# Kernel tuning notes

Measured on AMD Instinct MI355X. Metric: run time of the kernel, lower is better.

The kernel has to match this reference:

```python
import jax, jax.numpy as jnp
import numpy as np

B, LF, RATE = 2, 2048, 4
DF, DS, H = 1024, 1024, 8
D2 = DF // 2            # 512: both self (d1) and cross (d2) branch dims (equal split)
POOL_H = 2048
TS = LF // RATE         # 512 slow steps


def _p(key, shape):
    return jax.random.normal(key, shape, jnp.float32) * 0.02


def setup_inputs() -> dict:
    keys = iter(jax.random.split(jax.random.key(0), 32))
    inp = {
        "x_fast": jax.random.normal(next(keys), (B, LF, DF), jnp.float32),
        "x_slow": jax.random.normal(next(keys), (B, TS, DS), jnp.float32),
    }
    for name in ("fself", "fcross", "sself", "scross"):
        inp[f"{name}_wqkv"] = _p(next(keys), (D2, 3 * D2))
        inp[f"{name}_bqkv"] = jnp.zeros((3 * D2,), jnp.float32)
        inp[f"{name}_wo"] = _p(next(keys), (D2, D2))
        inp[f"{name}_bo"] = jnp.zeros((D2,), jnp.float32)
    inp["lift_w"] = _p(next(keys), (DS, D2))
    inp["lift_b"] = jnp.zeros((D2,), jnp.float32)
    inp["pool_w1"] = _p(next(keys), (RATE * DF, POOL_H))
    inp["pool_b1"] = jnp.zeros((POOL_H,), jnp.float32)
    inp["pool_w2"] = _p(next(keys), (POOL_H, D2))
    inp["pool_b2"] = jnp.zeros((D2,), jnp.float32)
    return inp


def _mha(q_in, k_in, v_in, wqkv, bqkv, wo, bo):
    """Standard multihead attention with fused in-proj weight [d, 3d]."""
    b, tq, d = q_in.shape
    hd = d // H
    q = q_in @ wqkv[:, :d] + bqkv[:d]
    k = k_in @ wqkv[:, d:2 * d] + bqkv[d:2 * d]
    v = v_in @ wqkv[:, 2 * d:] + bqkv[2 * d:]
    q = q.reshape(b, tq, H, hd)
    k = k.reshape(b, k_in.shape[1], H, hd)
    v = v.reshape(b, v_in.shape[1], H, hd)
    scores = jnp.einsum('bqhd,bkhd->bhqk', q, k) * np.float32(1.0 / np.sqrt(hd))
    w = jax.nn.softmax(scores, axis=-1)
    o = jnp.einsum('bhqk,bkhd->bqhd', w, v).reshape(b, tq, d)
    return o @ wo + bo


def _forward(x_fast, x_slow,
             fself_wqkv, fself_bqkv, fself_wo, fself_bo,
             fcross_wqkv, fcross_bqkv, fcross_wo, fcross_bo,
             sself_wqkv, sself_bqkv, sself_wo, sself_bo,
             scross_wqkv, scross_bqkv, scross_wo, scross_bo,
             lift_w, lift_b, pool_w1, pool_b1, pool_w2, pool_b2):
    b = x_fast.shape[0]
    # ---- fast level: lift slow -> fast timescale (ffn applied before repeat)
    y = jnp.repeat(x_slow @ lift_w + lift_b, RATE, axis=1)          # [B, LF, D2]
    x1, x2 = x_fast[..., :D2], x_fast[..., D2:]
    z_fast = jnp.concatenate([
        _mha(x1, x1, x1, fself_wqkv, fself_bqkv, fself_wo, fself_bo),
        _mha(x2, y, y, fcross_wqkv, fcross_bqkv, fcross_wo, fcross_bo),
    ], axis=-1)
    # ---- slow level: causal block pooling of fast sequence
    blocks = x_fast.reshape(b, TS, RATE * DF)                        # LF == TS*RATE
    s = jax.nn.gelu(blocks @ pool_w1 + pool_b1) @ pool_w2 + pool_b2  # [B, TS, D2]
    # causal shift: prepend zero slow step, drop last (zero in pooled feature dim)
    s = jnp.concatenate([jnp.zeros((b, 1, D2), s.dtype), s[:, :-1]], axis=1)
    s1, s2 = x_slow[..., :D2], x_slow[..., D2:]
    z_slow = jnp.concatenate([
        _mha(s1, s1, s1, sself_wqkv, sself_bqkv, sself_wo, sself_bo),
        _mha(s2, s, s, scross_wqkv, scross_bqkv, scross_wo, scross_bo),
    ], axis=-1)
    return z_fast, z_slow


def reference(x_fast, x_slow,
              fself_wqkv, fself_bqkv, fself_wo, fself_bo,
              fcross_wqkv, fcross_bqkv, fcross_wo, fcross_bo,
              sself_wqkv, sself_bqkv, sself_wo, sself_bo,
              scross_wqkv, scross_bqkv, scross_wo, scross_bo,
              lift_w, lift_b, pool_w1, pool_b1, pool_w2, pool_b2):
    return _forward(x_fast, x_slow,
                    fself_wqkv, fself_bqkv, fself_wo, fself_bo,
                    fcross_wqkv, fcross_bqkv, fcross_wo, fcross_bo,
                    sself_wqkv, sself_bqkv, sself_wo, sself_bo,
                    scross_wqkv, scross_bqkv, scross_wo, scross_bo,
                    lift_w, lift_b, pool_w1, pool_b1, pool_w2, pool_b2)
```

## Files before the change

kernel.cpp:

```cpp
#include <hip/hip_runtime.h>
#include <hip/hip_bf16.h>


typedef __attribute__((ext_vector_type(8))) short bf16x8;
typedef __attribute__((ext_vector_type(4))) float f32x4;
typedef unsigned short u16;
typedef unsigned int u32;

__device__ inline u16 f2bf(float f) {
    __hip_bfloat16 h = __float2bfloat16(f);
    return *reinterpret_cast<u16*>(&h);
}
__device__ inline u32 pack2(float a, float b) {
    return (u32)f2bf(a) | ((u32)f2bf(b) << 16);
}
__device__ inline void gld16(const u16* g, u16* l) {
    __builtin_amdgcn_global_load_lds(
        (const __attribute__((address_space(1))) void*)(g),
        (__attribute__((address_space(3))) void*)(l), 16, 0, 0);
}

struct GDesc {
    const u16* A; const u16* Bt; const float* bias;
    void* out0; u16* aux0; u16* aux1;
    int lda, ldb, ldc, K, ntx, mode, rshift, tile_end;
};
struct GPack { int n; int pad[3]; GDesc d[8]; };

template <int TMT>
__global__ __launch_bounds__(256)
void gemm_multi(GPack pk)
{
    constexpr int TM = TMT * 16;
    constexpr int W = TMT / 2;
    __shared__ u16 As[TM * 64];
    __shared__ u16 Bs[TM * 64];

    int bid = blockIdx.x;
    int di = 0;
    while (bid >= pk.d[di].tile_end) ++di;
    const GDesc g = pk.d[di];
    const int base = di ? pk.d[di - 1].tile_end : 0;
    const int local = bid - base;
    const int ty = local / g.ntx, tx = local - ty * g.ntx;
    const int row0 = ty * TM, col0 = tx * TM;

    const int t = threadIdx.x;
    const int wave = t >> 6, lane = t & 63;
    const int l15 = lane & 15, quad = lane >> 4;
    const int wm = (wave >> 1) * W * 16, wn = (wave & 1) * W * 16;

    const int srow = wave * 8 + (lane >> 3);
    const int scol = (lane & 7) * 8;
    const u16* Ag = g.A + (long long)(row0 + srow) * g.lda + scol;
    const u16* Bg = g.Bt + (long long)(col0 + srow) * g.ldb + scol;

    f32x4 acc[W][W];
#pragma unroll
    for (int i = 0; i < W; ++i)
#pragma unroll
        for (int j = 0; j < W; ++j) {
            acc[i][j][0] = 0.f; acc[i][j][1] = 0.f;
            acc[i][j][2] = 0.f; acc[i][j][3] = 0.f;
        }

    for (int k0 = 0; k0 < g.K; k0 += 64) {
        __syncthreads();
#pragma unroll
        for (int r = 0; r < TM / 32; ++r) {
            gld16(Ag + (long long)r * 32 * g.lda + k0, As + r * 2048 + wave * 512);
            gld16(Bg + (long long)r * 32 * g.ldb + k0, Bs + r * 2048 + wave * 512);
        }
        __syncthreads();
#pragma unroll
        for (int kc = 0; kc < 2; ++kc) {
            bf16x8 af[W], bfr[W];
#pragma unroll
            for (int i = 0; i < W; ++i) {
                af[i]  = *(const bf16x8*)(As + (wm + i * 16 + l15) * 64 + kc * 32 + quad * 8);
                bfr[i] = *(const bf16x8*)(Bs + (wn + i * 16 + l15) * 64 + kc * 32 + quad * 8);
            }
#pragma unroll
            for (int i = 0; i < W; ++i)
#pragma unroll
                for (int j = 0; j < W; ++j)
                    acc[i][j] = __builtin_amdgcn_mfma_f32_16x16x32_bf16(af[i], bfr[j], acc[i][j], 0, 0, 0);
        }
    }

    const int rmask = (1 << g.rshift) - 1;
#pragma unroll
    for (int i = 0; i < W; ++i)
#pragma unroll
        for (int j = 0; j < W; ++j)
#pragma unroll
            for (int r = 0; r < 4; ++r) {
                int m = row0 + wm + i * 16 + quad * 4 + r;
                int n = col0 + wn + j * 16 + l15;
                float v = acc[i][j][r] + g.bias[n];
                if (g.mode == 0) {
                    ((float*)g.out0)[(long long)m * g.ldc + n] = v;
                } else if (g.mode == 1) {
                    ((u16*)g.out0)[(long long)m * g.ldc + n] = f2bf(v);
                } else if (g.mode == 2) {
                    float x3 = v * v * v;
                    v = 0.5f * v * (1.f + tanhf(0.7978845608028654f * (v + 0.044715f * x3)));
                    ((u16*)g.out0)[(long long)m * g.ldc + n] = f2bf(v);
                } else if (g.mode == 3) {
                    u16 h = f2bf(v);
                    if (n < 512) ((u16*)g.out0)[(long long)m * 512 + n] = h;
                    else if (n < 1024) g.aux0[(long long)m * 512 + (n - 512)] = h;
                    else {
                        int d = n - 1024;
                        int bb = m >> g.rshift, rr = m & rmask;
                        g.aux1[((long long)((bb * 8 + (d >> 6)) * 64 + (d & 63)) << g.rshift) + rr] = h;
                    }
                } else if (g.mode == 4) {
                    u16 h = f2bf(v);
                    if (n < 512) ((u16*)g.out0)[(long long)m * 512 + n] = h;
                    else {
                        int d = n - 512;
                        int bb = m >> g.rshift, rr = m & rmask;
                        g.aux1[((long long)((bb * 8 + (d >> 6)) * 64 + (d & 63)) << g.rshift) + rr] = h;
                    }
                } else {
                    int t9 = m & 511;
                    if (t9 != 511) ((u16*)g.out0)[(long long)(m + 1) * g.ldc + n] = f2bf(v);
                    if (t9 == 0)  ((u16*)g.out0)[(long long)m * g.ldc + n] = 0;
                }
            }
}

#define ALD 72

struct ADesc { const u16* Q; const u16* K; const u16* Vt; u16* O; int Rq, nk, tile_end, pad; };
struct APack { int n; int pad[3]; ADesc d[4]; };

__global__ __launch_bounds__(256)
void attn_multi(APack pk, float prescale)
{
    __shared__ u16 Qs[64 * 64];
    __shared__ u16 Ks[64 * 64];
    __shared__ u16 Vts[64 * 64];
    __shared__ u16 Ps[4][16 * ALD];

    int bid = blockIdx.x;
    int di = 0;
    while (bid >= pk.d[di].tile_end) ++di;
    const ADesc g = pk.d[di];
    const int base = di ? pk.d[di - 1].tile_end : 0;
    const int local = bid - base;

    const int t = threadIdx.x;
    const int wave = t >> 6, lane = t & 63;
    const int l15 = lane & 15, quad = lane >> 4;
    const int bh = local & 15, b = bh >> 3, h = bh & 7;
    const int q0 = (local >> 4) * 64;
    const int nk = g.nk;

    const int srow = wave * 8 + (lane >> 3);
    const int scol = (lane & 7) * 8;

    const u16* Qg = g.Q + ((long long)(b * g.Rq + q0 + srow) << 9) + h * 64 + scol;
    const u16* Kg = g.K + ((long long)(b * nk + srow) << 9) + h * 64 + scol;
    const u16* Vg = g.Vt + (long long)bh * 64 * nk + (long long)srow * nk + scol;

#pragma unroll
    for (int r = 0; r < 2; ++r)
        gld16(Qg + ((long long)r * 32 << 9), Qs + r * 2048 + wave * 512);
    __syncthreads();

    bf16x8 qf[2];
    qf[0] = *(const bf16x8*)(Qs + (wave * 16 + l15) * 64 + quad * 8);
    qf[1] = *(const bf16x8*)(Qs + (wave * 16 + l15) * 64 + 32 + quad * 8);

    f32x4 Oacc[4];
#pragma unroll
    for (int nt = 0; nt < 4; ++nt) { Oacc[nt][0] = 0.f; Oacc[nt][1] = 0.f; Oacc[nt][2] = 0.f; Oacc[nt][3] = 0.f; }
    float lr[4] = {0.f, 0.f, 0.f, 0.f};

    u16* Pw = &Ps[wave][0];

    for (int kt = 0; kt < nk; kt += 64) {
        __syncthreads();
#pragma unroll
        for (int r = 0; r < 2; ++r) {
            gld16(Kg + ((long long)(kt + r * 32) << 9), Ks + r * 2048 + wave * 512);
            gld16(Vg + (long long)r * 32 * nk + kt, Vts + r * 2048 + wave * 512);
        }
        __syncthreads();

#pragma unroll
        for (int k16 = 0; k16 < 4; ++k16) {
            f32x4 s;
            s[0] = 0.f; s[1] = 0.f; s[2] = 0.f; s[3] = 0.f;
            bf16x8 kf0 = *(const bf16x8*)(Ks + (k16 * 16 + l15) * 64 + quad * 8);
            bf16x8 kf1 = *(const bf16x8*)(Ks + (k16 * 16 + l15) * 64 + 32 + quad * 8);
            s = __builtin_amdgcn_mfma_f32_16x16x32_bf16(qf[0], kf0, s, 0, 0, 0);
            s = __builtin_amdgcn_mfma_f32_16x16x32_bf16(qf[1], kf1, s, 0, 0, 0);
#pragma unroll
            for (int r = 0; r < 4; ++r) {
                float p = exp2f(s[r] * prescale);
                lr[r] += p;
                Pw[(quad * 4 + r) * ALD + k16 * 16 + l15] = f2bf(p);
            }
        }

        bf16x8 pf0 = *(const bf16x8*)(Pw + l15 * ALD + quad * 8);
        bf16x8 pf1 = *(const bf16x8*)(Pw + l15 * ALD + 32 + quad * 8);
#pragma unroll
        for (int nt = 0; nt < 4; ++nt) {
            bf16x8 vf0 = *(const bf16x8*)(Vts + (nt * 16 + l15) * 64 + quad * 8);
            bf16x8 vf1 = *(const bf16x8*)(Vts + (nt * 16 + l15) * 64 + 32 + quad * 8);
            Oacc[nt] = __builtin_amdgcn_mfma_f32_16x16x32_bf16(pf0, vf0, Oacc[nt], 0, 0, 0);
            Oacc[nt] = __builtin_amdgcn_mfma_f32_16x16x32_bf16(pf1, vf1, Oacc[nt], 0, 0, 0);
        }
    }

    float inv[4];
#pragma unroll
    for (int r = 0; r < 4; ++r) {
        float s = lr[r];
#pragma unroll
        for (int off = 1; off < 16; off <<= 1) s += __shfl_xor(s, off);
        inv[r] = 1.f / s;
    }

    u16* Ob = g.O + ((long long)(b * g.Rq + q0 + wave * 16 + quad * 4) << 9) + h * 64;
#pragma unroll
    for (int nt = 0; nt < 4; ++nt)
#pragma unroll
        for (int r = 0; r < 4; ++r)
            Ob[(long long)r * 512 + nt * 16 + l15] = f2bf(Oacc[nt][r] * inv[r]);
}

struct WDesc { const float* src; u16* dst; int ldn, K, tx_, tile_end; };
struct WPack { int n; int pad[3]; WDesc d[12]; };

__global__ __launch_bounds__(256)
void wt_multi(WPack pk)
{
    __shared__ float T[64][68];
    int bid = blockIdx.x;
    int di = 0;
    while (bid >= pk.d[di].tile_end) ++di;
    const WDesc g = pk.d[di];
    const int base = di ? pk.d[di - 1].tile_end : 0;
    const int local = bid - base;
    const int k0 = (local % g.tx_) * 64;
    const int n0 = (local / g.tx_) * 64;
    const int t = threadIdx.x;
#pragma unroll
    for (int i = 0; i < 4; ++i) {
        int idx = t + i * 256;
        int r = idx >> 4, c4 = idx & 15;
        float4 v = *(const float4*)(g.src + (long long)(k0 + r) * g.ldn + n0 + c4 * 4);
        T[r][c4 * 4 + 0] = v.x; T[r][c4 * 4 + 1] = v.y;
        T[r][c4 * 4 + 2] = v.z; T[r][c4 * 4 + 3] = v.w;
    }
    __syncthreads();
#pragma unroll
    for (int i = 0; i < 4; ++i) {
        int idx = t + i * 256;
        int rn = idx >> 4, k4 = idx & 15;
        uint2 u;
        u.x = pack2(T[k4 * 4 + 0][rn], T[k4 * 4 + 1][rn]);
        u.y = pack2(T[k4 * 4 + 2][rn], T[k4 * 4 + 3][rn]);
        *(uint2*)(g.dst + (long long)(n0 + rn) * g.K + k0 + k4 * 4) = u;
    }
}

__global__ __launch_bounds__(256)
void c_cvt2(const float* __restrict__ a, u16* __restrict__ da, int na8,
            const float* __restrict__ b, u16* __restrict__ db)
{
    int i = blockIdx.x * 256 + threadIdx.x;
    const float* s; u16* d;
    if (i < na8) { s = a + (long long)i * 8; d = da + (long long)i * 8; }
    else { s = b + (long long)(i - na8) * 8; d = db + (long long)(i - na8) * 8; }
    float4 x = *(const float4*)s;
    float4 y = *(const float4*)(s + 4);
    uint4 u;
    u.x = pack2(x.x, x.y); u.y = pack2(x.z, x.w);
    u.z = pack2(y.x, y.y); u.w = pack2(y.z, y.w);
    *(uint4*)d = u;
}

extern "C" void kernel_launch(void* const* d_in, const int* in_sizes, int n_in,
                              void* d_out, int out_size, void* d_ws, size_t ws_size,
                              hipStream_t stream)
{
    const float* x_fast      = (const float*)d_in[0];
    const float* x_slow      = (const float*)d_in[1];
    const float* fself_wqkv  = (const float*)d_in[2];
    const float* fself_bqkv  = (const float*)d_in[3];
    const float* fself_wo    = (const float*)d_in[4];
    const float* fself_bo    = (const float*)d_in[5];
    const float* fcross_wqkv = (const float*)d_in[6];
    const float* fcross_bqkv = (const float*)d_in[7];
    const float* fcross_wo   = (const float*)d_in[8];
    const float* fcross_bo   = (const float*)d_in[9];
    const float* sself_wqkv  = (const float*)d_in[10];
    const float* sself_bqkv  = (const float*)d_in[11];
    const float* sself_wo    = (const float*)d_in[12];
    const float* sself_bo    = (const float*)d_in[13];
    const float* scross_wqkv = (const float*)d_in[14];
    const float* scross_bqkv = (const float*)d_in[15];
    const float* scross_wo   = (const float*)d_in[16];
    const float* scross_bo   = (const float*)d_in[17];
    const float* lift_w      = (const float*)d_in[18];
    const float* lift_b      = (const float*)d_in[19];
    const float* pool_w1     = (const float*)d_in[20];
    const float* pool_b1     = (const float*)d_in[21];
    const float* pool_w2     = (const float*)d_in[22];
    const float* pool_b2     = (const float*)d_in[23];

    float* out = (float*)d_out;
    float* zf = out;
    float* zs = out + 2LL * 2048 * 1024;

    float* ws = (float*)d_ws;
    u16* pw1T     = (u16*)(ws + 0);
    u16* wqkvT_f  = (u16*)(ws + 4194304);
    u16* wqkvT_c  = (u16*)(ws + 4587520);
    u16* wqkvT_s  = (u16*)(ws + 4980736);
    u16* wqkvT_sc = (u16*)(ws + 5373952);
    u16* liftT    = (u16*)(ws + 5767168);
    u16* pw2T     = (u16*)(ws + 6029312);
    u16* woT_f    = (u16*)(ws + 6553600);
    u16* woT_c    = (u16*)(ws + 6684672);
    u16* woT_s    = (u16*)(ws + 6815744);
    u16* woT_sc   = (u16*)(ws + 6946816);
    u16* xfb      = (u16*)(ws + 7077888);
    u16* xsb      = (u16*)(ws + 9175040);
    u16* q1       = (u16*)(ws + 9699328);
    u16* k1       = (u16*)(ws + 10747904);
    u16* vt1      = (u16*)(ws + 11796480);
    u16* qs       = (u16*)(ws + 12845056);
    u16* ks       = (u16*)(ws + 13107200);
    u16* vts      = (u16*)(ws + 13369344);
    u16* qcs      = (u16*)(ws + 13631488);
    u16* k2    = (u16*)(ws + 0);
    u16* vt2   = (u16*)(ws + 262144);
    u16* sbufS = (u16*)(ws + 524288);
    u16* kcs   = (u16*)(ws + 786432);
    u16* vtcs  = (u16*)(ws + 1048576);
    u16* fo1   = (u16*)(ws + 1310720);
    u16* fo2   = (u16*)(ws + 2359296);
    u16* so1   = (u16*)(ws + 3407872);
    u16* so2   = (u16*)(ws + 3670016);
    u16* q2   = (u16*)(out + 0);
    u16* ybuf = (u16*)(out + 1048576);
    u16* hbuf = (u16*)(out + 1310720);

    hipLaunchKernelGGL(c_cvt2, dim3(2560), dim3(256), 0, stream,
                       x_fast, xfb, 524288, x_slow, xsb);

    {
        WPack p; p.n = 11;
        int te = 0, i = 0;
        auto add = [&](const float* s, u16* d, int ldn, int K, int N) {
            te += (K / 64) * (N / 64);
            p.d[i++] = WDesc{s, d, ldn, K, K / 64, te};
        };
        add(pool_w1, pw1T, 2048, 4096, 2048);
        add(fself_wqkv, wqkvT_f, 1536, 512, 1536);
        add(fcross_wqkv, wqkvT_c, 1536, 512, 1536);
        add(sself_wqkv, wqkvT_s, 1536, 512, 1536);
        add(scross_wqkv, wqkvT_sc, 1536, 512, 1536);
        add(lift_w, liftT, 512, 1024, 512);
        add(pool_w2, pw2T, 512, 2048, 512);
        add(fself_wo, woT_f, 512, 512, 512);
        add(fcross_wo, woT_c, 512, 512, 512);
        add(sself_wo, woT_s, 512, 512, 512);
        add(scross_wo, woT_sc, 512, 512, 512);
        hipLaunchKernelGGL(wt_multi, dim3(te), dim3(256), 0, stream, p);
    }

    auto gl = [&](GPack& p, int i, const u16* A, int lda,
                  const u16* Bt, int ldb, const float* bias,
                  void* out0, int ldc, int M, int N, int K, int mode,
                  u16* aux0, u16* aux1, int rshift, int TM, int& te) {
        te += (M / TM) * (N / TM);
        p.d[i] = GDesc{A, Bt, bias, out0, aux0, aux1,
                       lda, ldb, ldc, K, N / TM, mode, rshift, te};
    };

    {
        GPack p; p.n = 6; int te = 0;
        gl(p, 0, xfb, 4096, pw1T, 4096, pool_b1, hbuf, 2048,
           1024, 2048, 4096, 2, 0, 0, 0, 128, te);
        gl(p, 1, xfb, 1024, wqkvT_f, 512, fself_bqkv, q1, 512,
           4096, 1536, 512, 3, k1, vt1, 11, 128, te);
        gl(p, 2, xfb + 512, 1024, wqkvT_c, 512, fcross_bqkv, q2, 512,
           4096, 512, 512, 1, 0, 0, 0, 128, te);
        gl(p, 3, xsb, 1024, wqkvT_s, 512, sself_bqkv, qs, 512,
           1024, 1536, 512, 3, ks, vts, 9, 128, te);
        gl(p, 4, xsb, 1024, liftT, 1024, lift_b, ybuf, 512,
           1024, 512, 1024, 1, 0, 0, 0, 128, te);
        gl(p, 5, xsb + 512, 1024, wqkvT_sc, 512, scross_bqkv, qcs, 512,
           1024, 512, 512, 1, 0, 0, 0, 128, te);
        hipLaunchKernelGGL(gemm_multi<8>, dim3(te), dim3(256), 0, stream, p);
    }

    {
        GPack p; p.n = 2; int te = 0;
        gl(p, 0, ybuf, 512, wqkvT_c + 512 * 512, 512, fcross_bqkv + 512, k2, 512,
           1024, 1024, 512, 4, 0, vt2, 9, 64, te);
        gl(p, 1, hbuf, 2048, pw2T, 2048, pool_b2, sbufS, 512,
           1024, 512, 2048, 6, 0, 0, 0, 64, te);
        hipLaunchKernelGGL(gemm_multi<4>, dim3(te), dim3(256), 0, stream, p);
    }

    {
        GPack p; p.n = 1; int te = 0;
        gl(p, 0, sbufS, 512, wqkvT_sc + 512 * 512, 512, scross_bqkv + 512, kcs, 512,
           1024, 1024, 512, 4, 0, vtcs, 9, 64, te);
        hipLaunchKernelGGL(gemm_multi<4>, dim3(te), dim3(256), 0, stream, p);
    }

    {
        APack p; p.n = 4;
        int te = 0, i = 0;
        auto add = [&](const u16* Q, const u16* K, const u16* Vt, u16* O, int Rq, int nk) {
            te += (Rq / 64) * 16;
            p.d[i++] = ADesc{Q, K, Vt, O, Rq, nk, te, 0};
        };
        add(q1, k1, vt1, fo1, 2048, 2048);
        add(q2, k2, vt2, fo2, 2048, 512);
        add(qs, ks, vts, so1, 512, 512);
        add(qcs, kcs, vtcs, so2, 512, 512);
        hipLaunchKernelGGL(attn_multi, dim3(te), dim3(256), 0, stream, p,
                           0.125f * 1.4426950408889634f);
    }

    {
        GPack p; p.n = 4; int te = 0;
        gl(p, 0, fo1, 512, woT_f, 512, fself_bo, zf, 1024,
           4096, 512, 512, 0, 0, 0, 0, 128, te);
        gl(p, 1, fo2, 512, woT_c, 512, fcross_bo, zf + 512, 1024,
           4096, 512, 512, 0, 0, 0, 0, 128, te);
        gl(p, 2, so1, 512, woT_s, 512, sself_bo, zs, 1024,
           1024, 512, 512, 0, 0, 0, 0, 128, te);
        gl(p, 3, so2, 512, woT_sc, 512, scross_bo, zs + 512, 1024,
           1024, 512, 512, 0, 0, 0, 0, 128, te);
        hipLaunchKernelGGL(gemm_multi<8>, dim3(te), dim3(256), 0, stream, p);
    }
}
```

Baseline: 390.9 us.

## Split-K the pooling GEMM with a GELU reduce kernel and XOR-swizzle LDS tiles

The long K=4096 pooling GEMM is split into two K=2048 halves that run as separate tile groups in the batched GEMM launch, writing bf16 partials without bias. A new gelu_sum kernel adds the partials and bias and applies GELU. This shortens the tail of the tile scheduling in the batched launch at the cost of an extra kernel and extra bf16 partial traffic, with the sum now rounded from bf16 partials. LDS tiles in the GEMM and attention kernels also get an XOR column swizzle, which is meant to cut bank conflicts on fragment reads.

After: 374.1 us. -4.3%, faster.

```diff
diff --git a/kernel.cpp b/kernel.cpp
--- a/kernel.cpp
+++ b/kernel.cpp
@@ -13,6 +13,11 @@
 }
 __device__ inline u32 pack2(float a, float b) {
     return (u32)f2bf(a) | ((u32)f2bf(b) << 16);
+}
+__device__ inline float bf2f(u16 h) {
+    u32 x = ((u32)h) << 16; float f;
+    __builtin_memcpy(&f, &x, 4);
+    return f;
 }
 __device__ inline void gld16(const u16* g, u16* l) {
     __builtin_amdgcn_global_load_lds(
@@ -51,9 +56,11 @@
     const int wm = (wave >> 1) * W * 16, wn = (wave & 1) * W * 16;
 
     const int srow = wave * 8 + (lane >> 3);
-    const int scol = (lane & 7) * 8;
-    const u16* Ag = g.A + (long long)(row0 + srow) * g.lda + scol;
-    const u16* Bg = g.Bt + (long long)(col0 + srow) * g.ldb + scol;
+    const int ssw = (((lane & 7) ^ (lane >> 3))) * 8;
+    const u16* Ag = g.A + (long long)(row0 + srow) * g.lda + ssw;
+    const u16* Bg = g.Bt + (long long)(col0 + srow) * g.ldb + ssw;
+
+    const int c0 = (quad ^ (l15 & 7)) * 8;
 
     f32x4 acc[W][W];
 #pragma unroll
@@ -74,11 +81,12 @@
         __syncthreads();
 #pragma unroll
         for (int kc = 0; kc < 2; ++kc) {
+            const int cc = kc ? (c0 ^ 32) : c0;
             bf16x8 af[W], bfr[W];
 #pragma unroll
             for (int i = 0; i < W; ++i) {
-                af[i]  = *(const bf16x8*)(As + (wm + i * 16 + l15) * 64 + kc * 32 + quad * 8);
-                bfr[i] = *(const bf16x8*)(Bs + (wn + i * 16 + l15) * 64 + kc * 32 + quad * 8);
+                af[i]  = *(const bf16x8*)(As + (wm + i * 16 + l15) * 64 + cc);
+                bfr[i] = *(const bf16x8*)(Bs + (wn + i * 16 + l15) * 64 + cc);
             }
 #pragma unroll
             for (int i = 0; i < W; ++i)
@@ -97,10 +105,11 @@
             for (int r = 0; r < 4; ++r) {
                 int m = row0 + wm + i * 16 + quad * 4 + r;
                 int n = col0 + wn + j * 16 + l15;
-                float v = acc[i][j][r] + g.bias[n];
+                float v = acc[i][j][r];
+                if (g.mode != 5) v += g.bias[n];
                 if (g.mode == 0) {
                     ((float*)g.out0)[(long long)m * g.ldc + n] = v;
-                } else if (g.mode == 1) {
+                } else if (g.mode == 1 || g.mode == 5) {
                     ((u16*)g.out0)[(long long)m * g.ldc + n] = f2bf(v);
                 } else if (g.mode == 2) {
                     float x3 = v * v * v;
@@ -159,11 +168,12 @@
     const int nk = g.nk;
 
     const int srow = wave * 8 + (lane >> 3);
-    const int scol = (lane & 7) * 8;
-
-    const u16* Qg = g.Q + ((long long)(b * g.Rq + q0 + srow) << 9) + h * 64 + scol;
-    const u16* Kg = g.K + ((long long)(b * nk + srow) << 9) + h * 64 + scol;
-    const u16* Vg = g.Vt + (long long)bh * 64 * nk + (long long)srow * nk + scol;
+    const int ssw = (((lane & 7) ^ (lane >> 3))) * 8;
+    const int c0 = (quad ^ (l15 & 7)) * 8;
+
+    const u16* Qg = g.Q + ((long long)(b * g.Rq + q0 + srow) << 9) + h * 64 + ssw;
+    const u16* Kg = g.K + ((long long)(b * nk + srow) << 9) + h * 64 + ssw;
+    const u16* Vg = g.Vt + (long long)bh * 64 * nk + (long long)srow * nk + ssw;
 
 #pragma unroll
     for (int r = 0; r < 2; ++r)
@@ -171,8 +181,8 @@
     __syncthreads();
 
     bf16x8 qf[2];
-    qf[0] = *(const bf16x8*)(Qs + (wave * 16 + l15) * 64 + quad * 8);
-    qf[1] = *(const bf16x8*)(Qs + (wave * 16 + l15) * 64 + 32 + quad * 8);
+    qf[0] = *(const bf16x8*)(Qs + (wave * 16 + l15) * 64 + c0);
+    qf[1] = *(const bf16x8*)(Qs + (wave * 16 + l15) * 64 + (c0 ^ 32));
 
     f32x4 Oacc[4];
 #pragma unroll
@@ -194,8 +204,8 @@
         for (int k16 = 0; k16 < 4; ++k16) {
             f32x4 s;
             s[0] = 0.f; s[1] = 0.f; s[2] = 0.f; s[3] = 0.f;
-            bf16x8 kf0 = *(const bf16x8*)(Ks + (k16 * 16 + l15) * 64 + quad * 8);
-            bf16x8 kf1 = *(const bf16x8*)(Ks + (k16 * 16 + l15) * 64 + 32 + quad * 8);
+            bf16x8 kf0 = *(const bf16x8*)(Ks + (k16 * 16 + l15) * 64 + c0);
+            bf16x8 kf1 = *(const bf16x8*)(Ks + (k16 * 16 + l15) * 64 + (c0 ^ 32));
             s = __builtin_amdgcn_mfma_f32_16x16x32_bf16(qf[0], kf0, s, 0, 0, 0);
             s = __builtin_amdgcn_mfma_f32_16x16x32_bf16(qf[1], kf1, s, 0, 0, 0);
 #pragma unroll
@@ -210,8 +220,8 @@
         bf16x8 pf1 = *(const bf16x8*)(Pw + l15 * ALD + 32 + quad * 8);
 #pragma unroll
         for (int nt = 0; nt < 4; ++nt) {
-            bf16x8 vf0 = *(const bf16x8*)(Vts + (nt * 16 + l15) * 64 + quad * 8);
-            bf16x8 vf1 = *(const bf16x8*)(Vts + (nt * 16 + l15) * 64 + 32 + quad * 8);
+            bf16x8 vf0 = *(const bf16x8*)(Vts + (nt * 16 + l15) * 64 + c0);
+            bf16x8 vf1 = *(const bf16x8*)(Vts + (nt * 16 + l15) * 64 + (c0 ^ 32));
             Oacc[nt] = __builtin_amdgcn_mfma_f32_16x16x32_bf16(pf0, vf0, Oacc[nt], 0, 0, 0);
             Oacc[nt] = __builtin_amdgcn_mfma_f32_16x16x32_bf16(pf1, vf1, Oacc[nt], 0, 0, 0);
         }
@@ -284,6 +294,34 @@
     u.x = pack2(x.x, x.y); u.y = pack2(x.z, x.w);
     u.z = pack2(y.x, y.y); u.w = pack2(y.z, y.w);
     *(uint4*)d = u;
+}
+
+__global__ __launch_bounds__(256)
+void gelu_sum(u16* __restrict__ p0, const u16* __restrict__ p1,
+              const float* __restrict__ bias)
+{
+    int i8 = (blockIdx.x * 256 + threadIdx.x) * 8;
+    uint4 a = *(const uint4*)(p0 + i8);
+    uint4 b = *(const uint4*)(p1 + i8);
+    int n = i8 & 2047;
+    float4 bi0 = *(const float4*)(bias + n);
+    float4 bi1 = *(const float4*)(bias + n + 4);
+    float bb[8] = {bi0.x, bi0.y, bi0.z, bi0.w, bi1.x, bi1.y, bi1.z, bi1.w};
+    u32 aw[4] = {a.x, a.y, a.z, a.w};
+    u32 bw[4] = {b.x, b.y, b.z, b.w};
+    u32 ow[4];
+#pragma unroll
+    for (int k = 0; k < 4; ++k) {
+        float v0 = bf2f((u16)(aw[k] & 0xffff)) + bf2f((u16)(bw[k] & 0xffff)) + bb[2 * k];
+        float v1 = bf2f((u16)(aw[k] >> 16)) + bf2f((u16)(bw[k] >> 16)) + bb[2 * k + 1];
+        float x3 = v0 * v0 * v0;
+        v0 = 0.5f * v0 * (1.f + tanhf(0.7978845608028654f * (v0 + 0.044715f * x3)));
+        x3 = v1 * v1 * v1;
+        v1 = 0.5f * v1 * (1.f + tanhf(0.7978845608028654f * (v1 + 0.044715f * x3)));
+        ow[k] = pack2(v0, v1);
+    }
+    uint4 o; o.x = ow[0]; o.y = ow[1]; o.z = ow[2]; o.w = ow[3];
+    *(uint4*)(p0 + i8) = o;
 }
 
 extern "C" void kernel_launch(void* const* d_in, const int* in_sizes, int n_in,
@@ -352,6 +390,7 @@
     u16* q2   = (u16*)(out + 0);
     u16* ybuf = (u16*)(out + 1048576);
     u16* hbuf = (u16*)(out + 1310720);
+    u16* p1b  = (u16*)(out + 2359296);
 
     hipLaunchKernelGGL(c_cvt2, dim3(2560), dim3(256), 0, stream,
                        x_fast, xfb, 524288, x_slow, xsb);
@@ -387,21 +426,25 @@
     };
 
     {
-        GPack p; p.n = 6; int te = 0;
+        GPack p; p.n = 7; int te = 0;
         gl(p, 0, xfb, 4096, pw1T, 4096, pool_b1, hbuf, 2048,
-           1024, 2048, 4096, 2, 0, 0, 0, 128, te);
-        gl(p, 1, xfb, 1024, wqkvT_f, 512, fself_bqkv, q1, 512,
+           1024, 2048, 2048, 5, 0, 0, 0, 128, te);
+        gl(p, 1, xfb + 2048, 4096, pw1T + 2048, 4096, pool_b1, p1b, 2048,
+           1024, 2048, 2048, 5, 0, 0, 0, 128, te);
+        gl(p, 2, xfb, 1024, wqkvT_f, 512, fself_bqkv, q1, 512,
            4096, 1536, 512, 3, k1, vt1, 11, 128, te);
-        gl(p, 2, xfb + 512, 1024, wqkvT_c, 512, fcross_bqkv, q2, 512,
+        gl(p, 3, xfb + 512, 1024, wqkvT_c, 512, fcross_bqkv, q2, 512,
            4096, 512, 512, 1, 0, 0, 0, 128, te);
-        gl(p, 3, xsb, 1024, wqkvT_s, 512, sself_bqkv, qs, 512,
+        gl(p, 4, xsb, 1024, wqkvT_s, 512, sself_bqkv, qs, 512,
            1024, 1536, 512, 3, ks, vts, 9, 128, te);
-        gl(p, 4, xsb, 1024, liftT, 1024, lift_b, ybuf, 512,
+        gl(p, 5, xsb, 1024, liftT, 1024, lift_b, ybuf, 512,
            1024, 512, 1024, 1, 0, 0, 0, 128, te);
-        gl(p, 5, xsb + 512, 1024, wqkvT_sc, 512, scross_bqkv, qcs, 512,
+        gl(p, 6, xsb + 512, 1024, wqkvT_sc, 512, scross_bqkv, qcs, 512,
            1024, 512, 512, 1, 0, 0, 0, 128, te);
         hipLaunchKernelGGL(gemm_multi<8>, dim3(te), dim3(256), 0, stream, p);
     }
+
+    hipLaunchKernelGGL(gelu_sum, dim3(1024), dim3(256), 0, stream, hbuf, p1b, pool_b1);
 
     {
         GPack p; p.n = 2; int te = 0;
```
